# Kernel optimization log

Measured on AMD Instinct MI355X. Metric: run time of the kernel, lower is better.

The kernel has to match this reference:

```python
import jax, jax.numpy as jnp
import numpy as np

BN_EPS = 1e-5
CLUSTER_SIZE = 32  # K (real clusters kept after softmax)


def setup_inputs() -> dict:
    key = jax.random.key(0)
    ks = jax.random.split(key, 7)
    B, N, D, Ktot, K = 4096, 128, 512, 48, 32
    x = jax.random.normal(ks[0], (B, N, D), dtype=jnp.float32)
    clusters = jax.random.normal(ks[1], (D, Ktot), dtype=jnp.float32) / np.sqrt(D)
    bn_w = jax.random.uniform(ks[2], (Ktot,), dtype=jnp.float32)
    bn_b = jax.random.normal(ks[3], (Ktot,), dtype=jnp.float32)
    bn_rm = jax.random.normal(ks[4], (Ktot,), dtype=jnp.float32)
    bn_rv = jax.random.uniform(ks[5], (Ktot,), dtype=jnp.float32)  # positive variance
    clusters2 = jax.random.normal(ks[6], (1, D, K), dtype=jnp.float32) / np.sqrt(D)
    return {"x": x, "clusters": clusters, "bn_w": bn_w, "bn_b": bn_b,
            "bn_rm": bn_rm, "bn_rv": bn_rv, "clusters2": clusters2}


def reference(x, clusters, bn_w, bn_b, bn_rm, bn_rv, clusters2):
    # x: [B, N, D]; clusters: [D, Ktot]; clusters2: [1, D, K]
    B, N, D = x.shape
    K = clusters2.shape[-1]
    # cluster projection: [B, N, Ktot]
    logits = jnp.einsum('bnd,dk->bnk', x, clusters)
    # inference BatchNorm1d (affine with running stats)
    inv_std = jax.lax.rsqrt(bn_rv + BN_EPS)
    logits = (logits - bn_rm) * inv_std * bn_w + bn_b
    # softmax over real + ghost clusters, then drop ghost (no renorm)
    assignment = jax.nn.softmax(logits, axis=-1)[..., :K]  # [B, N, K]
    a_sum = jnp.sum(assignment, axis=1, keepdims=True)      # [B, 1, K]
    a = a_sum * clusters2                                   # [B, D, K]
    # weighted VLAD accumulate: [B, D, K]
    vlad = jnp.einsum('bnk,bnd->bdk', assignment, x) - a
    # intra-normalize (L2 across descriptor dim D, per cluster)
    vlad = vlad / jnp.maximum(jnp.linalg.norm(vlad, axis=1, keepdims=True), 1e-12)
    # flatten and L2-normalize full vector
    vlad = vlad.reshape(B, D * K)
    vlad = vlad / jnp.maximum(jnp.linalg.norm(vlad, axis=1, keepdims=True), 1e-12)
    return vlad
```

## Files before the change

### kernel.cpp

```cpp
#include <hip/hip_runtime.h>

typedef unsigned short u16;
typedef unsigned int u32;
typedef __attribute__((ext_vector_type(8))) short short8;
typedef __attribute__((ext_vector_type(4))) float f32x4;
typedef __attribute__((ext_vector_type(4))) u32 u32x4;
typedef __attribute__((ext_vector_type(2))) u32 u32x2;

#define NPT 128
#define DIM 512
#define KT 48
#define KC 32
#define BPB 16

__device__ __forceinline__ u16 f2bf(float f) {
    unsigned u = __builtin_bit_cast(unsigned, f);
    return (u16)((u + 0x7FFFu + ((u >> 16) & 1u)) >> 16);
}

__device__ __forceinline__ u32 cvtpk(float lo, float hi) {
    u32 r;
    asm("v_cvt_pk_bf16_f32 %0, %1, %2" : "=v"(r) : "v"(lo), "v"(hi));
    return r;
}

__device__ __forceinline__ int swz(int n) {
    return ((n & 7) ^ ((n >> 3) & 7)) << 4;
}

__global__ void prep_kernel(const float* __restrict__ clusters,
                            const float* __restrict__ bn_w,
                            const float* __restrict__ bn_b,
                            const float* __restrict__ bn_rm,
                            const float* __restrict__ bn_rv,
                            u16* __restrict__ cTs,
                            float* __restrict__ tvec) {
    const int k = blockIdx.x;
    const float s = bn_w[k] * rsqrtf(bn_rv[k] + 1e-5f);
    if (threadIdx.x == 0) tvec[k] = bn_b[k] - bn_rm[k] * s;
    for (int d = threadIdx.x; d < DIM; d += blockDim.x)
        cTs[k * DIM + d] = f2bf(clusters[d * KT + k] * s);
}

__global__ __launch_bounds__(512)
void vlad_kernel(const float* __restrict__ x,
                 const float* __restrict__ c2,
                 const u16* __restrict__ cTs,
                 const float* __restrict__ tvec,
                 float* __restrict__ out) {
    __shared__ __align__(16) u16 xs[NPT * DIM];
    __shared__ __align__(16) u16 aT[KC][136];
    __shared__ float asum_part[8][KC];
    __shared__ float colsq_part[8][KC];

    const int tid  = threadIdx.x;
    const int wave = tid >> 6;
    const int lane = tid & 63;
    const int lr   = lane & 15;
    const int lg   = lane >> 4;

    const int b0i = blockIdx.x * BPB;

    const float t0 = tvec[lr], t1 = tvec[16 + lr], t2 = tvec[32 + lr];

    {
        const float* gxw = x + (size_t)b0i * (NPT * DIM) + (wave * 16) * DIM;
        #pragma unroll
        for (int bt = 0; bt < 4; ++bt) {
            f32x4 tmp[8];
            #pragma unroll
            for (int i = 0; i < 8; ++i) {
                int it = bt * 8 + i;
                tmp[i] = *(const f32x4*)(gxw + (it >> 1) * DIM + (it & 1) * 256 + lane * 4);
            }
            #pragma unroll
            for (int i = 0; i < 8; ++i) {
                int it = bt * 8 + i;
                int r = wave * 16 + (it >> 1);
                u32x2 w2;
                w2[0] = cvtpk(tmp[i][0], tmp[i][1]);
                w2[1] = cvtpk(tmp[i][2], tmp[i][3]);
                int off = ((it & 1) * 512 + lane * 8) ^ swz(r);
                *(u32x2*)((char*)xs + r * 1024 + off) = w2;
            }
        }
    }

    for (int m = 0; m < BPB; ++m) {
        const int bm = b0i + m;

        f32x4 acc0 = {0.f,0.f,0.f,0.f}, acc1 = {0.f,0.f,0.f,0.f}, acc2 = {0.f,0.f,0.f,0.f};
        {
            const int nrow = wave * 16 + lr;
            const int rowbase = nrow * 1024;
            const int sw = swz(nrow);
            #pragma unroll 2
            for (int step = 0; step < 16; ++step) {
                const int d0 = step * 32 + lg * 8;
                short8 af = *(const short8*)((const char*)xs + (rowbase + ((2 * d0) ^ sw)));
                short8 bb0 = *(const short8*)(cTs + (0 * 16 + lr) * DIM + d0);
                short8 bb1 = *(const short8*)(cTs + (1 * 16 + lr) * DIM + d0);
                short8 bb2 = *(const short8*)(cTs + (2 * 16 + lr) * DIM + d0);
                acc0 = __builtin_amdgcn_mfma_f32_16x16x32_bf16(af, bb0, acc0, 0, 0, 0);
                acc1 = __builtin_amdgcn_mfma_f32_16x16x32_bf16(af, bb1, acc1, 0, 0, 0);
                acc2 = __builtin_amdgcn_mfma_f32_16x16x32_bf16(af, bb2, acc2, 0, 0, 0);
            }
        }
        {
            float a0[4], a1[4];
            #pragma unroll
            for (int r = 0; r < 4; ++r) {
                float l0 = acc0[r] + t0, l1 = acc1[r] + t1, l2 = acc2[r] + t2;
                float mx = fmaxf(fmaxf(l0, l1), l2);
                #pragma unroll
                for (int o = 1; o < 16; o <<= 1) mx = fmaxf(mx, __shfl_xor(mx, o));
                float e0 = __expf(l0 - mx), e1 = __expf(l1 - mx), e2 = __expf(l2 - mx);
                float s = e0 + e1 + e2;
                #pragma unroll
                for (int o = 1; o < 16; o <<= 1) s += __shfl_xor(s, o);
                float inv = 1.0f / s;
                a0[r] = e0 * inv; a1[r] = e1 * inv;
            }
            float p0 = 0.f, p1 = 0.f;
            #pragma unroll
            for (int r = 0; r < 4; ++r) {
                int n = wave * 16 + lg * 4 + r;
                aT[lr][n]      = f2bf(a0[r]);
                aT[16 + lr][n] = f2bf(a1[r]);
                p0 += a0[r]; p1 += a1[r];
            }
            p0 += __shfl_xor(p0, 16); p0 += __shfl_xor(p0, 32);
            p1 += __shfl_xor(p1, 16); p1 += __shfl_xor(p1, 32);
            if (lane < 16) { asum_part[wave][lane] = p0; asum_part[wave][16 + lane] = p1; }
        }
        __syncthreads();

        const int pm = (m + 1 < BPB) ? bm + 1 : bm;
        const float* nx = x + (size_t)pm * (NPT * DIM) + (wave * 16) * DIM;
        u32x4 stg[16];
        f32x4 vacc[4][2];
        #pragma unroll
        for (int i = 0; i < 4; ++i) {
            vacc[i][0] = (f32x4){0.f,0.f,0.f,0.f};
            vacc[i][1] = (f32x4){0.f,0.f,0.f,0.f};
        }
        #pragma unroll
        for (int ns = 0; ns < 4; ++ns) {
            f32x4 t[8];
            #pragma unroll
            for (int rr = 0; rr < 4; ++rr) {
                int i = ns * 4 + rr;
                t[2 * rr]     = *(const f32x4*)(nx + i * DIM + lane * 8);
                t[2 * rr + 1] = *(const f32x4*)(nx + i * DIM + lane * 8 + 4);
            }
            short8 bf0 = *(const short8*)(&aT[lr][ns * 32 + lg * 8]);
            short8 bf1 = *(const short8*)(&aT[16 + lr][ns * 32 + lg * 8]);
            const int n0 = ns * 32 + lg * 8;
            const int q  = (ns * 4 + lg) & 7;
            const char* pbase = (const char*)xs + n0 * 1024;
            #pragma unroll
            for (int dti = 0; dti < 4; ++dti) {
                const int d = (wave * 4 + dti) * 16 + lr;
                const int twod = 2 * d;
                short8 af;
                #pragma unroll
                for (int j = 0; j < 8; ++j)
                    af[j] = *(const short*)(pbase + j * 1024 + (twod ^ ((j ^ q) << 4)));
                vacc[dti][0] = __builtin_amdgcn_mfma_f32_16x16x32_bf16(af, bf0, vacc[dti][0], 0, 0, 0);
                vacc[dti][1] = __builtin_amdgcn_mfma_f32_16x16x32_bf16(af, bf1, vacc[dti][1], 0, 0, 0);
            }
            #pragma unroll
            for (int rr = 0; rr < 4; ++rr) {
                int i = ns * 4 + rr;
                u32x4 w;
                w[0] = cvtpk(t[2 * rr][0],     t[2 * rr][1]);
                w[1] = cvtpk(t[2 * rr][2],     t[2 * rr][3]);
                w[2] = cvtpk(t[2 * rr + 1][0], t[2 * rr + 1][1]);
                w[3] = cvtpk(t[2 * rr + 1][2], t[2 * rr + 1][3]);
                stg[i] = w;
            }
        }
        __syncthreads();

        #pragma unroll
        for (int i = 0; i < 16; ++i) {
            int r = wave * 16 + i;
            *(u32x4*)((char*)xs + r * 1024 + ((lane * 16) ^ swz(r))) = stg[i];
        }

        float as0 = 0.f, as1 = 0.f;
        #pragma unroll
        for (int w2 = 0; w2 < 8; ++w2) {
            as0 += asum_part[w2][lr];
            as1 += asum_part[w2][16 + lr];
        }
        float cs0 = 0.f, cs1 = 0.f;
        #pragma unroll
        for (int dti = 0; dti < 4; ++dti) {
            #pragma unroll
            for (int r = 0; r < 4; ++r) {
                int d = (wave * 4 + dti) * 16 + lg * 4 + r;
                float v0 = vacc[dti][0][r] - as0 * c2[d * KC + lr];
                float v1 = vacc[dti][1][r] - as1 * c2[d * KC + 16 + lr];
                vacc[dti][0][r] = v0; vacc[dti][1][r] = v1;
                cs0 += v0 * v0; cs1 += v1 * v1;
            }
        }
        cs0 += __shfl_xor(cs0, 16); cs0 += __shfl_xor(cs0, 32);
        cs1 += __shfl_xor(cs1, 16); cs1 += __shfl_xor(cs1, 32);
        if (lane < 16) { colsq_part[wave][lane] = cs0; colsq_part[wave][16 + lane] = cs1; }
        __syncthreads();
        float sq0 = 0.f, sq1 = 0.f;
        #pragma unroll
        for (int w2 = 0; w2 < 8; ++w2) {
            sq0 += colsq_part[w2][lr];
            sq1 += colsq_part[w2][16 + lr];
        }
        float cn0 = sqrtf(sq0), cn1 = sqrtf(sq1);
        float s10 = 1.0f / fmaxf(cn0, 1e-12f);
        float s11 = 1.0f / fmaxf(cn1, 1e-12f);
        float c10 = cn0 * s10, c11 = cn1 * s11;
        float tot = c10 * c10 + c11 * c11;
        #pragma unroll
        for (int o = 1; o < 16; o <<= 1) tot += __shfl_xor(tot, o);
        float gs = 1.0f / fmaxf(sqrtf(tot), 1e-12f);
        float sk0 = s10 * gs, sk1 = s11 * gs;
        {
            float* ob = out + (size_t)bm * (DIM * KC);
            #pragma unroll
            for (int dti = 0; dti < 4; ++dti) {
                #pragma unroll
                for (int r = 0; r < 4; ++r) {
                    int d = (wave * 4 + dti) * 16 + lg * 4 + r;
                    ob[d * KC + lr]      = vacc[dti][0][r] * sk0;
                    ob[d * KC + 16 + lr] = vacc[dti][1][r] * sk1;
                }
            }
        }
    }
}

extern "C" void kernel_launch(void* const* d_in, const int* in_sizes, int n_in,
                              void* d_out, int out_size, void* d_ws, size_t ws_size,
                              hipStream_t stream) {
    const float* x        = (const float*)d_in[0];
    const float* clusters = (const float*)d_in[1];
    const float* bn_w     = (const float*)d_in[2];
    const float* bn_b     = (const float*)d_in[3];
    const float* bn_rm    = (const float*)d_in[4];
    const float* bn_rv    = (const float*)d_in[5];
    const float* c2       = (const float*)d_in[6];
    float* out = (float*)d_out;

    u16*   cTs  = (u16*)d_ws;
    float* tvec = (float*)((char*)d_ws + KT * DIM * sizeof(u16));

    const int B = in_sizes[0] / (NPT * DIM);

    prep_kernel<<<KT, 256, 0, stream>>>(clusters, bn_w, bn_b, bn_rm, bn_rv, cTs, tvec);
    vlad_kernel<<<B / BPB, 512, 0, stream>>>(x, c2, cTs, tvec, out);
}
```

Baseline: 406.2 us.

## Stream x in 16-row double-buffered LDS chunks and stage cluster weights in LDS

```diff
diff --git a/kernel.cpp b/kernel.cpp
--- a/kernel.cpp
+++ b/kernel.cpp
@@ -5,7 +5,6 @@
 typedef __attribute__((ext_vector_type(8))) short short8;
 typedef __attribute__((ext_vector_type(4))) float f32x4;
 typedef __attribute__((ext_vector_type(4))) u32 u32x4;
-typedef __attribute__((ext_vector_type(2))) u32 u32x2;
 
 #define NPT 128
 #define DIM 512
@@ -22,6 +21,11 @@
     u32 r;
     asm("v_cvt_pk_bf16_f32 %0, %1, %2" : "=v"(r) : "v"(lo), "v"(hi));
     return r;
+}
+
+__device__ __forceinline__ void lds_barrier() {
+    asm volatile("s_waitcnt lgkmcnt(0)" ::: "memory");
+    __builtin_amdgcn_s_barrier();
 }
 
 __device__ __forceinline__ int swz(int n) {
@@ -48,7 +52,8 @@
                  const u16* __restrict__ cTs,
                  const float* __restrict__ tvec,
                  float* __restrict__ out) {
-    __shared__ __align__(16) u16 xs[NPT * DIM];
+    __shared__ __align__(16) u16 cTsL[KT * DIM];
+    __shared__ __align__(16) u16 buf[2][16 * DIM];
     __shared__ __align__(16) u16 aT[KC][136];
     __shared__ float asum_part[8][KC];
     __shared__ float colsq_part[8][KC];
@@ -60,52 +65,110 @@
     const int lg   = lane >> 4;
 
     const int b0i = blockIdx.x * BPB;
+    const float* xblk = x + (size_t)b0i * (NPT * DIM);
 
     const float t0 = tvec[lr], t1 = tvec[16 + lr], t2 = tvec[32 + lr];
 
+    const int srow = tid >> 5;
+    const int scol = (tid & 31) * 16;
+    const int sbyte = scol * 2;
+    const int ssw = swz(srow);
+
+    #pragma unroll
+    for (int i = 0; i < 6; ++i) {
+        int idx = tid + i * 512;
+        int k = idx >> 6, slot = idx & 63;
+        u32x4 v = *(const u32x4*)(cTs + k * DIM + slot * 8);
+        *(u32x4*)((char*)cTsL + k * 1024 + ((slot * 16) ^ swz(k))) = v;
+    }
     {
-        const float* gxw = x + (size_t)b0i * (NPT * DIM) + (wave * 16) * DIM;
-        #pragma unroll
-        for (int bt = 0; bt < 4; ++bt) {
-            f32x4 tmp[8];
-            #pragma unroll
-            for (int i = 0; i < 8; ++i) {
-                int it = bt * 8 + i;
-                tmp[i] = *(const f32x4*)(gxw + (it >> 1) * DIM + (it & 1) * 256 + lane * 4);
-            }
-            #pragma unroll
-            for (int i = 0; i < 8; ++i) {
-                int it = bt * 8 + i;
-                int r = wave * 16 + (it >> 1);
-                u32x2 w2;
-                w2[0] = cvtpk(tmp[i][0], tmp[i][1]);
-                w2[1] = cvtpk(tmp[i][2], tmp[i][3]);
-                int off = ((it & 1) * 512 + lane * 8) ^ swz(r);
-                *(u32x2*)((char*)xs + r * 1024 + off) = w2;
-            }
-        }
+        const float* g = xblk + srow * DIM + scol;
+        f32x4 a0 = *(const f32x4*)(g);
+        f32x4 a1 = *(const f32x4*)(g + 4);
+        f32x4 a2 = *(const f32x4*)(g + 8);
+        f32x4 a3 = *(const f32x4*)(g + 12);
+        u32x4 wA, wB;
+        wA[0] = cvtpk(a0[0], a0[1]); wA[1] = cvtpk(a0[2], a0[3]);
+        wA[2] = cvtpk(a1[0], a1[1]); wA[3] = cvtpk(a1[2], a1[3]);
+        wB[0] = cvtpk(a2[0], a2[1]); wB[1] = cvtpk(a2[2], a2[3]);
+        wB[2] = cvtpk(a3[0], a3[1]); wB[3] = cvtpk(a3[2], a3[3]);
+        char* dst = (char*)buf[0] + srow * 1024;
+        *(u32x4*)(dst + (sbyte ^ ssw)) = wA;
+        *(u32x4*)(dst + ((sbyte + 16) ^ ssw)) = wB;
     }
+    __syncthreads();
 
     for (int m = 0; m < BPB; ++m) {
-        const int bm = b0i + m;
-
         f32x4 acc0 = {0.f,0.f,0.f,0.f}, acc1 = {0.f,0.f,0.f,0.f}, acc2 = {0.f,0.f,0.f,0.f};
-        {
-            const int nrow = wave * 16 + lr;
-            const int rowbase = nrow * 1024;
-            const int sw = swz(nrow);
-            #pragma unroll 2
-            for (int step = 0; step < 16; ++step) {
-                const int d0 = step * 32 + lg * 8;
-                short8 af = *(const short8*)((const char*)xs + (rowbase + ((2 * d0) ^ sw)));
-                short8 bb0 = *(const short8*)(cTs + (0 * 16 + lr) * DIM + d0);
-                short8 bb1 = *(const short8*)(cTs + (1 * 16 + lr) * DIM + d0);
-                short8 bb2 = *(const short8*)(cTs + (2 * 16 + lr) * DIM + d0);
-                acc0 = __builtin_amdgcn_mfma_f32_16x16x32_bf16(af, bb0, acc0, 0, 0, 0);
-                acc1 = __builtin_amdgcn_mfma_f32_16x16x32_bf16(af, bb1, acc1, 0, 0, 0);
-                acc2 = __builtin_amdgcn_mfma_f32_16x16x32_bf16(af, bb2, acc2, 0, 0, 0);
-            }
-        }
+        short8 af2[4][4];
+
+        #pragma unroll
+        for (int ns = 0; ns < 4; ++ns) {
+            #pragma unroll
+            for (int h = 0; h < 2; ++h) {
+                const int j = ns * 2 + h;
+                const int cur = j & 1;
+                const int gnext = m * 8 + j + 1;
+                const bool pOK = (gnext < BPB * 8);
+
+                f32x4 a0, a1, a2, a3;
+                if (pOK) {
+                    const float* g = xblk + (size_t)gnext * (16 * DIM) + srow * DIM + scol;
+                    a0 = *(const f32x4*)(g);
+                    a1 = *(const f32x4*)(g + 4);
+                    a2 = *(const f32x4*)(g + 8);
+                    a3 = *(const f32x4*)(g + 12);
+                }
+
+                if ((lane >> 5) == h) {
+                    const int nb = (lg & 1) * 8;
+                    #pragma unroll
+                    for (int dti = 0; dti < 4; ++dti) {
+                        const int dd = wave * 128 + dti * 32 + 2 * lr;
+                        short8 v;
+                        #pragma unroll
+                        for (int jj = 0; jj < 8; ++jj) {
+                            const int rr = nb + jj;
+                            v[jj] = *(const short*)((const char*)buf[cur] + rr * 1024 + (dd ^ swz(rr)));
+                        }
+                        af2[ns][dti] = v;
+                    }
+                }
+
+                if (wave == j) {
+                    const char* xb = (const char*)buf[cur] + lr * 1024;
+                    const int sw = swz(lr);
+                    const char* c0 = (const char*)cTsL + lr * 1024;
+                    const char* c1 = (const char*)cTsL + (16 + lr) * 1024;
+                    const char* c2p = (const char*)cTsL + (32 + lr) * 1024;
+                    const int s1 = swz(16 + lr), s2 = swz(32 + lr);
+                    #pragma unroll 2
+                    for (int step = 0; step < 16; ++step) {
+                        const int off = step * 64 + lg * 16;
+                        short8 af  = *(const short8*)(xb + (off ^ sw));
+                        short8 bb0 = *(const short8*)(c0 + (off ^ sw));
+                        short8 bb1 = *(const short8*)(c1 + (off ^ s1));
+                        short8 bb2 = *(const short8*)(c2p + (off ^ s2));
+                        acc0 = __builtin_amdgcn_mfma_f32_16x16x32_bf16(af, bb0, acc0, 0, 0, 0);
+                        acc1 = __builtin_amdgcn_mfma_f32_16x16x32_bf16(af, bb1, acc1, 0, 0, 0);
+                        acc2 = __builtin_amdgcn_mfma_f32_16x16x32_bf16(af, bb2, acc2, 0, 0, 0);
+                    }
+                }
+
+                if (pOK) {
+                    u32x4 wA, wB;
+                    wA[0] = cvtpk(a0[0], a0[1]); wA[1] = cvtpk(a0[2], a0[3]);
+                    wA[2] = cvtpk(a1[0], a1[1]); wA[3] = cvtpk(a1[2], a1[3]);
+                    wB[0] = cvtpk(a2[0], a2[1]); wB[1] = cvtpk(a2[2], a2[3]);
+                    wB[2] = cvtpk(a3[0], a3[1]); wB[3] = cvtpk(a3[2], a3[3]);
+                    char* dst = (char*)buf[cur ^ 1] + srow * 1024;
+                    *(u32x4*)(dst + (sbyte ^ ssw)) = wA;
+                    *(u32x4*)(dst + ((sbyte + 16) ^ ssw)) = wB;
+                }
+                lds_barrier();
+            }
+        }
+
         {
             float a0[4], a1[4];
             #pragma unroll
@@ -133,11 +196,8 @@
             p1 += __shfl_xor(p1, 16); p1 += __shfl_xor(p1, 32);
             if (lane < 16) { asum_part[wave][lane] = p0; asum_part[wave][16 + lane] = p1; }
         }
-        __syncthreads();
-
-        const int pm = (m + 1 < BPB) ? bm + 1 : bm;
-        const float* nx = x + (size_t)pm * (NPT * DIM) + (wave * 16) * DIM;
-        u32x4 stg[16];
+        lds_barrier();
+
         f32x4 vacc[4][2];
         #pragma unroll
         for (int i = 0; i < 4; ++i) {
@@ -146,46 +206,13 @@
         }
         #pragma unroll
         for (int ns = 0; ns < 4; ++ns) {
-            f32x4 t[8];
-            #pragma unroll
-            for (int rr = 0; rr < 4; ++rr) {
-                int i = ns * 4 + rr;
-                t[2 * rr]     = *(const f32x4*)(nx + i * DIM + lane * 8);
-                t[2 * rr + 1] = *(const f32x4*)(nx + i * DIM + lane * 8 + 4);
-            }
             short8 bf0 = *(const short8*)(&aT[lr][ns * 32 + lg * 8]);
             short8 bf1 = *(const short8*)(&aT[16 + lr][ns * 32 + lg * 8]);
-            const int n0 = ns * 32 + lg * 8;
-            const int q  = (ns * 4 + lg) & 7;
-            const char* pbase = (const char*)xs + n0 * 1024;
             #pragma unroll
             for (int dti = 0; dti < 4; ++dti) {
-                const int d = (wave * 4 + dti) * 16 + lr;
-                const int twod = 2 * d;
-                short8 af;
-                #pragma unroll
-                for (int j = 0; j < 8; ++j)
-                    af[j] = *(const short*)(pbase + j * 1024 + (twod ^ ((j ^ q) << 4)));
-                vacc[dti][0] = __builtin_amdgcn_mfma_f32_16x16x32_bf16(af, bf0, vacc[dti][0], 0, 0, 0);
-                vacc[dti][1] = __builtin_amdgcn_mfma_f32_16x16x32_bf16(af, bf1, vacc[dti][1], 0, 0, 0);
-            }
-            #pragma unroll
-            for (int rr = 0; rr < 4; ++rr) {
-                int i = ns * 4 + rr;
-                u32x4 w;
-                w[0] = cvtpk(t[2 * rr][0],     t[2 * rr][1]);
-                w[1] = cvtpk(t[2 * rr][2],     t[2 * rr][3]);
-                w[2] = cvtpk(t[2 * rr + 1][0], t[2 * rr + 1][1]);
-                w[3] = cvtpk(t[2 * rr + 1][2], t[2 * rr + 1][3]);
-                stg[i] = w;
-            }
-        }
-        __syncthreads();
-
-        #pragma unroll
-        for (int i = 0; i < 16; ++i) {
-            int r = wave * 16 + i;
-            *(u32x4*)((char*)xs + r * 1024 + ((lane * 16) ^ swz(r))) = stg[i];
+                vacc[dti][0] = __builtin_amdgcn_mfma_f32_16x16x32_bf16(af2[ns][dti], bf0, vacc[dti][0], 0, 0, 0);
+                vacc[dti][1] = __builtin_amdgcn_mfma_f32_16x16x32_bf16(af2[ns][dti], bf1, vacc[dti][1], 0, 0, 0);
+            }
         }
 
         float as0 = 0.f, as1 = 0.f;
@@ -209,7 +236,7 @@
         cs0 += __shfl_xor(cs0, 16); cs0 += __shfl_xor(cs0, 32);
         cs1 += __shfl_xor(cs1, 16); cs1 += __shfl_xor(cs1, 32);
         if (lane < 16) { colsq_part[wave][lane] = cs0; colsq_part[wave][16 + lane] = cs1; }
-        __syncthreads();
+        lds_barrier();
         float sq0 = 0.f, sq1 = 0.f;
         #pragma unroll
         for (int w2 = 0; w2 < 8; ++w2) {
@@ -226,7 +253,7 @@
         float gs = 1.0f / fmaxf(sqrtf(tot), 1e-12f);
         float sk0 = s10 * gs, sk1 = s11 * gs;
         {
-            float* ob = out + (size_t)bm * (DIM * KC);
+            float* ob = out + (size_t)(b0i + m) * (DIM * KC);
             #pragma unroll
             for (int dti = 0; dti < 4; ++dti) {
                 #pragma unroll
```

Measured after the change: 368.3 us. 1.1x faster.
